# Kernel tuning notes

Measured on AMD Instinct MI355X. Metric: run time of the kernel, lower is better.

## Reference

```python
import jax, jax.numpy as jnp
import numpy as np

B, N, S, C, H = 16, 64, 4096, 384, 6
DH = C // H
SCALE = DH ** -0.5


def setup_inputs() -> dict:
    k0 = jax.random.key(0)
    ks = jax.random.split(k0, 7)
    std = C ** -0.5
    return {
        "query": jax.random.normal(ks[0], (B, N, C), jnp.float32),
        "key": jax.random.normal(ks[1], (B, S, C), jnp.float32),
        "Wq": jax.random.normal(ks[2], (C, C), jnp.float32) * std,
        "Wk": jax.random.normal(ks[3], (C, C), jnp.float32) * std,
        "Wv": jax.random.normal(ks[4], (C, C), jnp.float32) * std,
        "Wp": jax.random.normal(ks[5], (C, C), jnp.float32) * std,
        "bp": jnp.zeros((C,), jnp.float32),
    }


def reference(query, key, Wq, Wk, Wv, Wp, bp):
    # q/k/v projections (no bias, matching qkv_bias=False); nn.Linear is x @ W.T
    q = (query @ Wq.T).reshape(B, N, H, DH).transpose(0, 2, 1, 3)  # [B,H,N,DH]
    k = (key @ Wk.T).reshape(B, S, H, DH).transpose(0, 2, 1, 3)    # [B,H,S,DH]
    v = (key @ Wv.T).reshape(B, S, H, DH).transpose(0, 2, 1, 3)    # [B,H,S,DH]

    attn = jnp.einsum('bhnd,bhsd->bhns', q, k) * SCALE  # [B,H,N,S]

    # hard_softmax over dim=-2 (the group/query axis): each key token is
    # hard-assigned (straight-through) to its argmax group.
    y_soft = jax.nn.softmax(attn, axis=-2)
    idx = jnp.argmax(y_soft, axis=-2)  # [B,H,S]
    y_hard = (jnp.arange(N)[:, None] == idx[..., None, :]).astype(attn.dtype)  # [B,H,N,S]
    a = y_hard + y_soft - jax.lax.stop_gradient(y_soft)

    # inv_attn renormalization over the key axis
    a = a / (a.sum(axis=-1, keepdims=True) + 1.0)

    out = jnp.einsum('bhns,bhsd->bhnd', a, v)            # [B,H,N,DH]
    out = out.transpose(0, 2, 1, 3).reshape(B, N, C)     # [B,N,C]
    return out @ Wp.T + bp
```

## Files before the change

kernel.cpp:

```cpp
#include <hip/hip_runtime.h>
#include <hip/hip_bf16.h>
#include <stdint.h>

#define B_ 16
#define N_ 64
#define S_ 4096
#define C_ 384
#define H_ 6
#define DH_ 64
#define SCALE_ 0.125f
#define TAU_ 2e-4f
#define LISTCAP 262144

typedef __attribute__((ext_vector_type(8))) short bf16x8;
typedef __attribute__((ext_vector_type(4))) float f32x4;
typedef __attribute__((ext_vector_type(4))) unsigned short u16x4;

static __device__ __forceinline__ unsigned short f2bf(float x) {
    union { float f; unsigned u; } v; v.f = x;
    unsigned r = v.u + 0x7FFFu + ((v.u >> 16) & 1u);
    return (unsigned short)(r >> 16);
}
static __device__ __forceinline__ float bf2f(unsigned short b) {
    union { unsigned u; float f; } v; v.u = ((unsigned)b) << 16; return v.f;
}
static __device__ __forceinline__ float bfu_lo(unsigned u) {
    union { unsigned u; float f; } v; v.u = u << 16; return v.f;
}
static __device__ __forceinline__ float bfu_hi(unsigned u) {
    union { unsigned u; float f; } v; v.u = u & 0xFFFF0000u; return v.f;
}

static __device__ __forceinline__ void gl_lds16(const void* g, void* l) {
    __builtin_amdgcn_global_load_lds(
        (const __attribute__((address_space(1))) unsigned int*)g,
        (__attribute__((address_space(3))) unsigned int*)l, 16, 0, 0);
}

#define PREP_BLOCKS 8192
#define QK_BLOCKS   (8 * H_ * B_)
#define TR_BLOCKS   72

#define TRT(r, c) sbuf[(r) * 65 + (c)]
#define WQS(d, c) sbuf[(d) * 49 + (c)]

__global__ __launch_bounds__(384) void prepqk_kernel(const float* __restrict__ key,
                                                     unsigned short* __restrict__ khi,
                                                     unsigned short* __restrict__ klo,
                                                     const float* __restrict__ query,
                                                     const float* __restrict__ Wq,
                                                     const float* __restrict__ Wk,
                                                     float* __restrict__ qk,
                                                     unsigned short* __restrict__ qkhi,
                                                     unsigned short* __restrict__ qklo,
                                                     const float* __restrict__ Wp,
                                                     const float* __restrict__ Wv,
                                                     float* __restrict__ wpT,
                                                     float* __restrict__ wvT) {
    __shared__ float qstage[8][C_];
    __shared__ float qv[8][DH_];
    __shared__ float sbuf[64 * 65];
    int t = threadIdx.x;
    if (blockIdx.x < PREP_BLOCKS) {
        size_t blk = (size_t)blockIdx.x * 3072;
#pragma unroll
        for (int half = 0; half < 2; ++half) {
            size_t base = blk + (size_t)half * 1536 + (size_t)t * 4;
            float4 x = *(const float4*)(key + base);
            float xs[4] = { x.x, x.y, x.z, x.w };
            unsigned short hi[4], lo[4];
#pragma unroll
            for (int i = 0; i < 4; ++i) {
                hi[i] = f2bf(xs[i]);
                lo[i] = f2bf(xs[i] - bf2f(hi[i]));
            }
            *(u16x4*)(khi + base) = *(u16x4*)hi;
            *(u16x4*)(klo + base) = *(u16x4*)lo;
        }
        return;
    }
    int e = blockIdx.x - PREP_BLOCKS;
    if (e >= QK_BLOCKS) {
        int e2 = e - QK_BLOCKS;
        const float* src = (e2 < 36) ? Wp : Wv;
        float* dst = (e2 < 36) ? wpT : wvT;
        int tile = e2 % 36;
        int r0 = (tile / 6) * 64, c0 = (tile % 6) * 64;
        if (t < 256) {
#pragma unroll
            for (int rep = 0; rep < 16; ++rep) {
                int idx = rep * 256 + t;
                int r = idx >> 6, c = idx & 63;
                TRT(r, c) = src[(size_t)(r0 + r) * C_ + c0 + c];
            }
        }
        __syncthreads();
        if (t < 256) {
#pragma unroll
            for (int rep = 0; rep < 16; ++rep) {
                int idx = rep * 256 + t;
                int rT = idx >> 6, cT = idx & 63;
                dst[(size_t)(c0 + rT) * C_ + r0 + cT] = TRT(cT, rT);
            }
        }
        return;
    }
    int ng = e & 7;
    int h = (e >> 3) % H_;
    int b = e / (8 * H_);
    int n0 = ng * 8;
#pragma unroll
    for (int i = 0; i < 8; ++i)
        qstage[i][t] = query[((size_t)(b * N_ + n0 + i)) * C_ + t];
    {
        int i0 = (t < 256) ? (t >> 6) : 0;
        int d = t & 63;
        float accA = 0.f, accB = 0.f;
        for (int c0 = 0; c0 < C_; c0 += 48) {
            __syncthreads();
#pragma unroll
            for (int rep = 0; rep < 8; ++rep) {
                int idx2 = rep * 384 + t;
                int r = idx2 / 48, c = idx2 % 48;
                WQS(r, c) = Wq[(size_t)(h * DH_ + r) * C_ + c0 + c];
            }
            __syncthreads();
            if (t < 256) {
#pragma unroll
                for (int cc = 0; cc < 48; cc += 4) {
                    accA += qstage[i0][c0 + cc + 0] * WQS(d, cc + 0)
                          + qstage[i0][c0 + cc + 1] * WQS(d, cc + 1)
                          + qstage[i0][c0 + cc + 2] * WQS(d, cc + 2)
                          + qstage[i0][c0 + cc + 3] * WQS(d, cc + 3);
                    accB += qstage[i0 + 4][c0 + cc + 0] * WQS(d, cc + 0)
                          + qstage[i0 + 4][c0 + cc + 1] * WQS(d, cc + 1)
                          + qstage[i0 + 4][c0 + cc + 2] * WQS(d, cc + 2)
                          + qstage[i0 + 4][c0 + cc + 3] * WQS(d, cc + 3);
                }
            }
        }
        if (t < 256) {
            qv[i0][d] = accA * SCALE_;
            qv[i0 + 4][d] = accB * SCALE_;
        }
    }
    __syncthreads();
    float a[8];
#pragma unroll
    for (int i = 0; i < 8; ++i) a[i] = 0.f;
    {
        const float* wk = Wk + (size_t)h * DH_ * C_ + t;
#pragma unroll 4
        for (int d = 0; d < DH_; ++d) {
            float w = wk[(size_t)d * C_];
#pragma unroll
            for (int i = 0; i < 8; ++i) a[i] += qv[i][d] * w;
        }
    }
#pragma unroll
    for (int i = 0; i < 8; ++i) qstage[i][t] = a[i];
    __syncthreads();
    {
        int r = t / 48, c0 = (t % 48) * 8;
        float v[8];
#pragma unroll
        for (int j = 0; j < 8; ++j) v[j] = qstage[r][c0 + j];
        unsigned short hi[8], lo[8];
#pragma unroll
        for (int j = 0; j < 8; ++j) {
            hi[j] = f2bf(v[j]);
            lo[j] = f2bf(v[j] - bf2f(hi[j]));
        }
        size_t o = ((size_t)(b * H_ + h) * N_ + n0 + r) * C_ + c0;
        float4 f0 = { v[0], v[1], v[2], v[3] };
        float4 f1 = { v[4], v[5], v[6], v[7] };
        *(float4*)(qk + o) = f0;
        *(float4*)(qk + o + 4) = f1;
        *(bf16x8*)(qkhi + o) = *(bf16x8*)hi;
        *(bf16x8*)(qklo + o) = *(bf16x8*)lo;
    }
}

__global__ __launch_bounds__(256) void attn_kernel(const unsigned short* __restrict__ qkhi,
                                                   const unsigned short* __restrict__ qklo,
                                                   const unsigned short* __restrict__ khi,
                                                   const unsigned short* __restrict__ klo,
                                                   unsigned int* __restrict__ idx,
                                                   unsigned int* __restrict__ flag_cnt,
                                                   unsigned int* __restrict__ flag_list) {
    __shared__ __align__(16) unsigned short sAhi[64 * 32];
    __shared__ __align__(16) unsigned short sAlo[64 * 32];
    __shared__ __align__(16) unsigned short sBhi[128 * 32];
    __shared__ __align__(16) unsigned short sBlo[128 * 32];
    int tid = threadIdx.x;
    int w = tid >> 6, l = tid & 63;
    int wm = w >> 1, wn = w & 1;
    int q4 = l >> 4, lm = l & 15;
    int s0 = blockIdx.x * 128;
    int h = blockIdx.y, b = blockIdx.z;
    size_t kbK = ((size_t)b * S_ + s0) * C_;
    size_t kbA = (size_t)(b * H_ + h) * N_ * C_;
    int trow16 = l >> 2;
    int tquart = ((l & 3) ^ ((l >> 3) & 3)) * 8;
    int sw = (q4 ^ ((lm >> 1) & 3)) * 8;

    f32x4 acc[2][4];
#pragma unroll
    for (int tm = 0; tm < 2; ++tm)
#pragma unroll
        for (int nt = 0; nt < 4; ++nt) acc[tm][nt] = (f32x4)0.f;

    for (int kc = 0; kc < C_; kc += 32) {
        __syncthreads();
#pragma unroll
        for (int i = 0; i < 6; ++i) {
            int gid = w * 6 + i;
            if (gid < 8) {
                gl_lds16(khi + kbK + (size_t)(gid * 16 + trow16) * C_ + kc + tquart,
                         (char*)sBhi + gid * 1024);
            } else if (gid < 16) {
                int g2 = gid - 8;
                gl_lds16(klo + kbK + (size_t)(g2 * 16 + trow16) * C_ + kc + tquart,
                         (char*)sBlo + g2 * 1024);
            } else if (gid < 20) {
                int g2 = gid - 16;
                gl_lds16(qkhi + kbA + (size_t)(g2 * 16 + trow16) * C_ + kc + tquart,
                         (char*)sAhi + g2 * 1024);
            } else {
                int g2 = gid - 20;
                gl_lds16(qklo + kbA + (size_t)(g2 * 16 + trow16) * C_ + kc + tquart,
                         (char*)sAlo + g2 * 1024);
            }
        }
        __syncthreads();
        bf16x8 ah[2], al[2];
#pragma unroll
        for (int tm = 0; tm < 2; ++tm) {
            int ar = (wm * 32 + tm * 16 + lm) * 32 + sw;
            ah[tm] = *(const bf16x8*)&sAhi[ar];
            al[tm] = *(const bf16x8*)&sAlo[ar];
        }
#pragma unroll
        for (int nt = 0; nt < 4; ++nt) {
            int nr = ((wn * 4 + nt) * 16 + lm) * 32 + sw;
            bf16x8 bh = *(const bf16x8*)&sBhi[nr];
            bf16x8 bl = *(const bf16x8*)&sBlo[nr];
#pragma unroll
            for (int tm = 0; tm < 2; ++tm) {
                acc[tm][nt] = __builtin_amdgcn_mfma_f32_16x16x32_bf16(ah[tm], bh, acc[tm][nt], 0, 0, 0);
                acc[tm][nt] = __builtin_amdgcn_mfma_f32_16x16x32_bf16(ah[tm], bl, acc[tm][nt], 0, 0, 0);
                acc[tm][nt] = __builtin_amdgcn_mfma_f32_16x16x32_bf16(al[tm], bh, acc[tm][nt], 0, 0, 0);
            }
        }
    }
    __syncthreads();

    float* rm1 = (float*)sBhi;
    float* rm2 = rm1 + 256;
    int* ri1 = (int*)(rm2 + 256);
    int* ri2 = ri1 + 256;

#pragma unroll
    for (int nt = 0; nt < 4; ++nt) {
        float m1 = -3.4e38f, m2 = -3.4e38f; int i1 = 0, i2 = 0;
#pragma unroll
        for (int tm = 0; tm < 2; ++tm)
#pragma unroll
            for (int r = 0; r < 4; ++r) {
                float v = acc[tm][nt][r];
                int row = wm * 32 + tm * 16 + q4 * 4 + r;
                if (v > m1) { m2 = m1; i2 = i1; m1 = v; i1 = row; }
                else if (v > m2) { m2 = v; i2 = row; }
            }
#pragma unroll
        for (int off = 16; off < 64; off <<= 1) {
            float om1 = __shfl_xor(m1, off), om2 = __shfl_xor(m2, off);
            int oi1 = __shfl_xor(i1, off), oi2 = __shfl_xor(i2, off);
            bool take = (om1 > m1) || (om1 == m1 && oi1 < i1);
            float w1 = take ? om1 : m1; int wi1 = take ? oi1 : i1;
            float l1 = take ? m1 : om1; int li1 = take ? i1 : oi1;
            float s2 = m2; int si2 = i2;
            if (om2 > s2) { s2 = om2; si2 = oi2; }
            if (l1 > s2) { s2 = l1; si2 = li1; }
            m1 = w1; i1 = wi1; m2 = s2; i2 = si2;
        }
        if (q4 == 0) {
            int cw = (wn * 4 + nt) * 16 + lm;
            rm1[wm * 128 + cw] = m1; rm2[wm * 128 + cw] = m2;
            ri1[wm * 128 + cw] = i1; ri2[wm * 128 + cw] = i2;
        }
    }
    __syncthreads();
    if (tid < 128) {
        float a1 = rm1[tid], a2 = rm2[tid];
        int ai1 = ri1[tid], ai2 = ri2[tid];
        float b1 = rm1[128 + tid], b2 = rm2[128 + tid];
        int bi1 = ri1[128 + tid], bi2 = ri2[128 + tid];
        float w1, s2; int wi1, wi2;
        if (b1 > a1) { w1 = b1; wi1 = bi1; s2 = a1; wi2 = ai1; if (b2 > s2) { s2 = b2; wi2 = bi2; } }
        else         { w1 = a1; wi1 = ai1; s2 = a2; wi2 = ai2; if (b1 > s2) { s2 = b1; wi2 = bi1; } }
        idx[(size_t)(b * H_ + h) * S_ + s0 + tid] = (unsigned)wi1;
        if (w1 - s2 < TAU_) {
            unsigned p = atomicAdd(flag_cnt, 1u);
            if (p < LISTCAP) {
                unsigned tok = (unsigned)((b * H_ + h) * S_ + s0 + tid);
                flag_list[p] = tok | ((unsigned)wi1 << 19) | ((unsigned)wi2 << 25);
            }
        }
    }
}

__global__ __launch_bounds__(256) void fixup_kernel(const float* __restrict__ qk,
                                                    const float* __restrict__ key,
                                                    const unsigned int* __restrict__ flag_list,
                                                    const unsigned int* __restrict__ flag_cnt,
                                                    unsigned int* __restrict__ idx) {
    int w = threadIdx.x >> 6, l = threadIdx.x & 63;
    unsigned total = flag_cnt[0];
    if (total > LISTCAP) total = LISTCAP;
    for (unsigned t = blockIdx.x * 4 + w; t < total; t += gridDim.x * 4) {
        unsigned e = flag_list[t];
        unsigned tok = e & 0x7FFFFu;
        int i1 = (int)((e >> 19) & 63u), i2 = (int)((e >> 25) & 63u);
        unsigned bh = tok >> 12;
        unsigned s = tok & 4095u;
        unsigned bb = bh / H_;
        int l32 = l & 31;
        const float* qrow = qk + ((size_t)bh * N_ + (l < 32 ? i1 : i2)) * C_ + l32 * 12;
        const float* krow = key + ((size_t)bb * S_ + s) * C_ + l32 * 12;
        float sum = 0.f;
#pragma unroll
        for (int c = 0; c < 12; ++c) sum += qrow[c] * krow[c];
#pragma unroll
        for (int off = 1; off < 32; off <<= 1) sum += __shfl_xor(sum, off);
        float d1 = __shfl(sum, 0);
        float d2 = __shfl(sum, 32);
        int win = (d2 > d1 || (d2 == d1 && i2 < i1)) ? i2 : i1;
        if (l == 0) idx[(size_t)bh * S_ + s] = (unsigned)win;
    }
}

__global__ __launch_bounds__(256) void hist_build_kernel(const unsigned int* __restrict__ idx,
                                                         unsigned int* __restrict__ offs,
                                                         unsigned int* __restrict__ order) {
    __shared__ unsigned int cnts[N_];
    __shared__ unsigned int pos[N_];
    int tid = threadIdx.x;
    int bh = blockIdx.x;
    if (tid < N_) cnts[tid] = 0u;
    __syncthreads();
    const unsigned int* idxp = idx + (size_t)bh * S_;
    for (int s = tid; s < S_; s += 256) atomicAdd(&cnts[idxp[s]], 1u);
    __syncthreads();
    if (tid < N_) {
        unsigned v = cnts[tid];
        unsigned x = v;
#pragma unroll
        for (int off = 1; off < 64; off <<= 1) {
            unsigned y = __shfl_up(x, off);
            if (tid >= off) x += y;
        }
        unsigned excl = x - v;
        pos[tid] = excl;
        offs[(size_t)bh * 65 + tid] = excl;
        if (tid == 63) offs[(size_t)bh * 65 + 64] = x;
    }
    __syncthreads();
    unsigned int* op = order + (size_t)bh * S_;
    for (int s = tid; s < S_; s += 256) {
        unsigned g = idxp[s];
        unsigned p = atomicAdd(&pos[g], 1u);
        op[p] = (unsigned)s;
    }
}

#define AGG_PARTS 8
__global__ __launch_bounds__(512) void aggv_kernel(const unsigned short* __restrict__ khi,
                                                   const unsigned int* __restrict__ order,
                                                   const unsigned int* __restrict__ offs,
                                                   const float* __restrict__ wvT,
                                                   float* __restrict__ gvn) {
    __shared__ float lrows[AGG_PARTS][C_];
    __shared__ float zrow[C_];
    __shared__ float pacc[AGG_PARTS][DH_];
    int tid = threadIdx.x;
    int part = tid >> 6, l = tid & 63;
    int h = blockIdx.y, b = blockIdx.z;
    int bh = b * H_ + h;
    int g = blockIdx.x;
    unsigned beg = offs[(size_t)bh * 65 + g];
    unsigned end = offs[(size_t)bh * 65 + g + 1];
    int cnt = (int)(end - beg);
    float inv = 1.f / ((float)cnt + 1.f);
    const unsigned int* op = order + (size_t)bh * S_ + beg;
    const unsigned int* kbase = (const unsigned int*)(khi + (size_t)b * S_ * C_);
    float a0 = 0.f, a1 = 0.f, a2 = 0.f, a3 = 0.f, a4 = 0.f, a5 = 0.f;
    for (int base = part * 64; base < cnt; base += 64 * AGG_PARTS) {
        int m = cnt - base; if (m > 64) m = 64;
        unsigned sv = (l < m) ? op[base + l] : 0u;
        int i = 0;
        for (; i + 8 <= m; i += 8) {
            int ss[8];
#pragma unroll
            for (int j = 0; j < 8; ++j) ss[j] = __shfl((int)sv, i + j);
            unsigned u[8][3];
#pragma unroll
            for (int j = 0; j < 8; ++j) {
                const unsigned int* kp = kbase + (size_t)ss[j] * (C_ / 2) + l * 3;
                u[j][0] = kp[0]; u[j][1] = kp[1]; u[j][2] = kp[2];
            }
#pragma unroll
            for (int j = 0; j < 8; ++j) {
                a0 += bfu_lo(u[j][0]); a1 += bfu_hi(u[j][0]);
                a2 += bfu_lo(u[j][1]); a3 += bfu_hi(u[j][1]);
                a4 += bfu_lo(u[j][2]); a5 += bfu_hi(u[j][2]);
            }
        }
        for (; i < m; ++i) {
            int s = (int)__shfl((int)sv, i);
            const unsigned int* kp = kbase + (size_t)s * (C_ / 2) + l * 3;
            unsigned u0 = kp[0], u1 = kp[1], u2 = kp[2];
            a0 += bfu_lo(u0); a1 += bfu_hi(u0);
            a2 += bfu_lo(u1); a3 += bfu_hi(u1);
            a4 += bfu_lo(u2); a5 += bfu_hi(u2);
        }
    }
    float* lp = &lrows[part][l * 6];
    lp[0] = a0 * inv; lp[1] = a1 * inv; lp[2] = a2 * inv;
    lp[3] = a3 * inv; lp[4] = a4 * inv; lp[5] = a5 * inv;
    __syncthreads();
    if (tid < C_) {
        float z = lrows[0][tid];
#pragma unroll
        for (int p = 1; p < AGG_PARTS; ++p) z += lrows[p][tid];
        zrow[tid] = z;
    }
    __syncthreads();
    {
        float a = 0.f;
        int cb = part * (C_ / AGG_PARTS);
#pragma unroll 8
        for (int cc = 0; cc < C_ / AGG_PARTS; ++cc) {
            int c = cb + cc;
            a += zrow[c] * wvT[(size_t)c * C_ + h * DH_ + l];
        }
        pacc[part][l] = a;
    }
    __syncthreads();
    if (part == 0) {
        float acc = pacc[0][l];
#pragma unroll
        for (int p = 1; p < AGG_PARTS; ++p) acc += pacc[p][l];
        gvn[((size_t)bh * N_ + g) * DH_ + l] = acc;
    }
}

__global__ __launch_bounds__(384) void out_kernel(const float* __restrict__ gvn,
                                                  const float* __restrict__ wpT,
                                                  const float* __restrict__ bp,
                                                  float* __restrict__ out) {
    __shared__ float vals[C_];
    int bn = blockIdx.x;
    int b = bn >> 6, n = bn & 63;
    int t = threadIdx.x;
    int h = t >> 6, d = t & 63;
    vals[t] = gvn[((size_t)(b * H_ + h) * N_ + n) * DH_ + d];
    __syncthreads();
    float s = bp[t];
#pragma unroll 8
    for (int c = 0; c < C_; ++c)
        s += vals[c] * wpT[(size_t)c * C_ + t];
    out[(size_t)bn * C_ + t] = s;
}

extern "C" void kernel_launch(void* const* d_in, const int* in_sizes, int n_in,
                              void* d_out, int out_size, void* d_ws, size_t ws_size,
                              hipStream_t stream) {
    (void)in_sizes; (void)n_in; (void)out_size; (void)ws_size;
    const float* query = (const float*)d_in[0];
    const float* key   = (const float*)d_in[1];
    const float* Wq    = (const float*)d_in[2];
    const float* Wk    = (const float*)d_in[3];
    const float* Wv    = (const float*)d_in[4];
    const float* Wp    = (const float*)d_in[5];
    const float* bp    = (const float*)d_in[6];
    float* out = (float*)d_out;

    char* ws = (char*)d_ws;
    size_t off = 0;
    unsigned short* khi  = (unsigned short*)(ws + off); off += (size_t)B_ * S_ * C_ * 2;
    unsigned short* klo  = (unsigned short*)(ws + off); off += (size_t)B_ * S_ * C_ * 2;
    float* qk            = (float*)(ws + off);          off += (size_t)B_ * H_ * N_ * C_ * 4;
    unsigned short* qkhi = (unsigned short*)(ws + off); off += (size_t)B_ * H_ * N_ * C_ * 2;
    unsigned short* qklo = (unsigned short*)(ws + off); off += (size_t)B_ * H_ * N_ * C_ * 2;
    unsigned int* idx    = (unsigned int*)(ws + off);   off += (size_t)B_ * H_ * S_ * 4;
    unsigned int* order  = (unsigned int*)(ws + off);   off += (size_t)B_ * H_ * S_ * 4;
    unsigned int* offs   = (unsigned int*)(ws + off);   off += (size_t)B_ * H_ * 65 * 4;
    float* gvn           = (float*)(ws + off);          off += (size_t)B_ * H_ * N_ * DH_ * 4;
    float* wpT           = (float*)(ws + off);          off += (size_t)C_ * C_ * 4;
    float* wvT           = (float*)(ws + off);          off += (size_t)C_ * C_ * 4;
    unsigned int* fcnt   = (unsigned int*)(ws + off);   off += 256;
    unsigned int* flist  = (unsigned int*)(ws + off);   off += (size_t)LISTCAP * 4;

    hipMemsetAsync(fcnt, 0, 256, stream);

    prepqk_kernel<<<PREP_BLOCKS + QK_BLOCKS + TR_BLOCKS, 384, 0, stream>>>(
        key, khi, klo, query, Wq, Wk, qk, qkhi, qklo, Wp, Wv, wpT, wvT);
    attn_kernel<<<dim3(S_ / 128, H_, B_), 256, 0, stream>>>(qkhi, qklo, khi, klo, idx, fcnt, flist);
    fixup_kernel<<<256, 256, 0, stream>>>(qk, key, flist, fcnt, idx);
    hist_build_kernel<<<B_ * H_, 256, 0, stream>>>(idx, offs, order);
    aggv_kernel<<<dim3(N_, H_, B_), 512, 0, stream>>>(khi, order, offs, wvT, gvn);
    out_kernel<<<B_ * N_, 384, 0, stream>>>(gvn, wpT, bp, out);
}
```

Baseline: 377.7 us.

## Fuse key bf16 hi/lo split into attention kernel, drop key prep pass

Result: no change. 384.1 us (+1.7%).

```diff
diff --git a/kernel.cpp b/kernel.cpp
--- a/kernel.cpp
+++ b/kernel.cpp
@@ -14,7 +14,6 @@
 
 typedef __attribute__((ext_vector_type(8))) short bf16x8;
 typedef __attribute__((ext_vector_type(4))) float f32x4;
-typedef __attribute__((ext_vector_type(4))) unsigned short u16x4;
 
 static __device__ __forceinline__ unsigned short f2bf(float x) {
     union { float f; unsigned u; } v; v.f = x;
@@ -24,12 +23,6 @@
 static __device__ __forceinline__ float bf2f(unsigned short b) {
     union { unsigned u; float f; } v; v.u = ((unsigned)b) << 16; return v.f;
 }
-static __device__ __forceinline__ float bfu_lo(unsigned u) {
-    union { unsigned u; float f; } v; v.u = u << 16; return v.f;
-}
-static __device__ __forceinline__ float bfu_hi(unsigned u) {
-    union { unsigned u; float f; } v; v.u = u & 0xFFFF0000u; return v.f;
-}
 
 static __device__ __forceinline__ void gl_lds16(const void* g, void* l) {
     __builtin_amdgcn_global_load_lds(
@@ -37,49 +30,27 @@
         (__attribute__((address_space(3))) unsigned int*)l, 16, 0, 0);
 }
 
-#define PREP_BLOCKS 8192
 #define QK_BLOCKS   (8 * H_ * B_)
 #define TR_BLOCKS   72
 
 #define TRT(r, c) sbuf[(r) * 65 + (c)]
 #define WQS(d, c) sbuf[(d) * 49 + (c)]
 
-__global__ __launch_bounds__(384) void prepqk_kernel(const float* __restrict__ key,
-                                                     unsigned short* __restrict__ khi,
-                                                     unsigned short* __restrict__ klo,
-                                                     const float* __restrict__ query,
-                                                     const float* __restrict__ Wq,
-                                                     const float* __restrict__ Wk,
-                                                     float* __restrict__ qk,
-                                                     unsigned short* __restrict__ qkhi,
-                                                     unsigned short* __restrict__ qklo,
-                                                     const float* __restrict__ Wp,
-                                                     const float* __restrict__ Wv,
-                                                     float* __restrict__ wpT,
-                                                     float* __restrict__ wvT) {
+__global__ __launch_bounds__(384) void qkT_kernel(const float* __restrict__ query,
+                                                  const float* __restrict__ Wq,
+                                                  const float* __restrict__ Wk,
+                                                  float* __restrict__ qk,
+                                                  unsigned short* __restrict__ qkhi,
+                                                  unsigned short* __restrict__ qklo,
+                                                  const float* __restrict__ Wp,
+                                                  const float* __restrict__ Wv,
+                                                  float* __restrict__ wpT,
+                                                  float* __restrict__ wvT) {
     __shared__ float qstage[8][C_];
     __shared__ float qv[8][DH_];
     __shared__ float sbuf[64 * 65];
     int t = threadIdx.x;
-    if (blockIdx.x < PREP_BLOCKS) {
-        size_t blk = (size_t)blockIdx.x * 3072;
-#pragma unroll
-        for (int half = 0; half < 2; ++half) {
-            size_t base = blk + (size_t)half * 1536 + (size_t)t * 4;
-            float4 x = *(const float4*)(key + base);
-            float xs[4] = { x.x, x.y, x.z, x.w };
-            unsigned short hi[4], lo[4];
-#pragma unroll
-            for (int i = 0; i < 4; ++i) {
-                hi[i] = f2bf(xs[i]);
-                lo[i] = f2bf(xs[i] - bf2f(hi[i]));
-            }
-            *(u16x4*)(khi + base) = *(u16x4*)hi;
-            *(u16x4*)(klo + base) = *(u16x4*)lo;
-        }
-        return;
-    }
-    int e = blockIdx.x - PREP_BLOCKS;
+    int e = blockIdx.x;
     if (e >= QK_BLOCKS) {
         int e2 = e - QK_BLOCKS;
         const float* src = (e2 < 36) ? Wp : Wv;
@@ -183,15 +154,13 @@
 
 __global__ __launch_bounds__(256) void attn_kernel(const unsigned short* __restrict__ qkhi,
                                                    const unsigned short* __restrict__ qklo,
-                                                   const unsigned short* __restrict__ khi,
-                                                   const unsigned short* __restrict__ klo,
+                                                   const float* __restrict__ key,
                                                    unsigned int* __restrict__ idx,
                                                    unsigned int* __restrict__ flag_cnt,
                                                    unsigned int* __restrict__ flag_list) {
+    __shared__ __align__(16) float sB[128 * 32];
     __shared__ __align__(16) unsigned short sAhi[64 * 32];
     __shared__ __align__(16) unsigned short sAlo[64 * 32];
-    __shared__ __align__(16) unsigned short sBhi[128 * 32];
-    __shared__ __align__(16) unsigned short sBlo[128 * 32];
     int tid = threadIdx.x;
     int w = tid >> 6, l = tid & 63;
     int wm = w >> 1, wn = w & 1;
@@ -203,6 +172,9 @@
     int trow16 = l >> 2;
     int tquart = ((l & 3) ^ ((l >> 3) & 3)) * 8;
     int sw = (q4 ^ ((lm >> 1) & 3)) * 8;
+    int swrow = l >> 3;
+    int swcol = ((l & 7) ^ (l >> 3)) * 4;
+    int sx = (lm & 7) << 4;
 
     f32x4 acc[2][4];
 #pragma unroll
@@ -215,13 +187,9 @@
 #pragma unroll
         for (int i = 0; i < 6; ++i) {
             int gid = w * 6 + i;
-            if (gid < 8) {
-                gl_lds16(khi + kbK + (size_t)(gid * 16 + trow16) * C_ + kc + tquart,
-                         (char*)sBhi + gid * 1024);
-            } else if (gid < 16) {
-                int g2 = gid - 8;
-                gl_lds16(klo + kbK + (size_t)(g2 * 16 + trow16) * C_ + kc + tquart,
-                         (char*)sBlo + g2 * 1024);
+            if (gid < 16) {
+                gl_lds16(key + kbK + (size_t)(gid * 8 + swrow) * C_ + kc + swcol,
+                         (char*)sB + gid * 1024);
             } else if (gid < 20) {
                 int g2 = gid - 16;
                 gl_lds16(qkhi + kbA + (size_t)(g2 * 16 + trow16) * C_ + kc + tquart,
@@ -242,9 +210,19 @@
         }
 #pragma unroll
         for (int nt = 0; nt < 4; ++nt) {
-            int nr = ((wn * 4 + nt) * 16 + lm) * 32 + sw;
-            bf16x8 bh = *(const bf16x8*)&sBhi[nr];
-            bf16x8 bl = *(const bf16x8*)&sBlo[nr];
+            int tr = (wn * 4 + nt) * 16 + lm;
+            const char* rowb = (const char*)sB + tr * 128;
+            float4 x0 = *(const float4*)(rowb + ((q4 * 32) ^ sx));
+            float4 x1 = *(const float4*)(rowb + ((q4 * 32 + 16) ^ sx));
+            float xs[8] = { x0.x, x0.y, x0.z, x0.w, x1.x, x1.y, x1.z, x1.w };
+            unsigned short hh[8], ll[8];
+#pragma unroll
+            for (int j = 0; j < 8; ++j) {
+                hh[j] = f2bf(xs[j]);
+                ll[j] = f2bf(xs[j] - bf2f(hh[j]));
+            }
+            bf16x8 bh = *(bf16x8*)hh;
+            bf16x8 bl = *(bf16x8*)ll;
 #pragma unroll
             for (int tm = 0; tm < 2; ++tm) {
                 acc[tm][nt] = __builtin_amdgcn_mfma_f32_16x16x32_bf16(ah[tm], bh, acc[tm][nt], 0, 0, 0);
@@ -255,7 +233,7 @@
     }
     __syncthreads();
 
-    float* rm1 = (float*)sBhi;
+    float* rm1 = (float*)sB;
     float* rm2 = rm1 + 256;
     int* ri1 = (int*)(rm2 + 256);
     int* ri2 = ri1 + 256;
@@ -340,9 +318,9 @@
     }
 }
 
-__global__ __launch_bounds__(256) void hist_build_kernel(const unsigned int* __restrict__ idx,
-                                                         unsigned int* __restrict__ offs,
-                                                         unsigned int* __restrict__ order) {
+__global__ __launch_bounds__(1024) void hist_build_kernel(const unsigned int* __restrict__ idx,
+                                                          unsigned int* __restrict__ offs,
+                                                          unsigned int* __restrict__ order) {
     __shared__ unsigned int cnts[N_];
     __shared__ unsigned int pos[N_];
     int tid = threadIdx.x;
@@ -350,7 +328,7 @@
     if (tid < N_) cnts[tid] = 0u;
     __syncthreads();
     const unsigned int* idxp = idx + (size_t)bh * S_;
-    for (int s = tid; s < S_; s += 256) atomicAdd(&cnts[idxp[s]], 1u);
+    for (int s = tid; s < S_; s += 1024) atomicAdd(&cnts[idxp[s]], 1u);
     __syncthreads();
     if (tid < N_) {
         unsigned v = cnts[tid];
@@ -367,7 +345,7 @@
     }
     __syncthreads();
     unsigned int* op = order + (size_t)bh * S_;
-    for (int s = tid; s < S_; s += 256) {
+    for (int s = tid; s < S_; s += 1024) {
         unsigned g = idxp[s];
         unsigned p = atomicAdd(&pos[g], 1u);
         op[p] = (unsigned)s;
@@ -375,7 +353,7 @@
 }
 
 #define AGG_PARTS 8
-__global__ __launch_bounds__(512) void aggv_kernel(const unsigned short* __restrict__ khi,
+__global__ __launch_bounds__(512) void aggv_kernel(const float* __restrict__ key,
                                                    const unsigned int* __restrict__ order,
                                                    const unsigned int* __restrict__ offs,
                                                    const float* __restrict__ wvT,
@@ -393,7 +371,7 @@
     int cnt = (int)(end - beg);
     float inv = 1.f / ((float)cnt + 1.f);
     const unsigned int* op = order + (size_t)bh * S_ + beg;
-    const unsigned int* kbase = (const unsigned int*)(khi + (size_t)b * S_ * C_);
+    const float* kbase = key + (size_t)b * S_ * C_;
     float a0 = 0.f, a1 = 0.f, a2 = 0.f, a3 = 0.f, a4 = 0.f, a5 = 0.f;
     for (int base = part * 64; base < cnt; base += 64 * AGG_PARTS) {
         int m = cnt - base; if (m > 64) m = 64;
@@ -403,26 +381,29 @@
             int ss[8];
 #pragma unroll
             for (int j = 0; j < 8; ++j) ss[j] = __shfl((int)sv, i + j);
-            unsigned u[8][3];
+            float2 u[8][3];
 #pragma unroll
             for (int j = 0; j < 8; ++j) {
-                const unsigned int* kp = kbase + (size_t)ss[j] * (C_ / 2) + l * 3;
-                u[j][0] = kp[0]; u[j][1] = kp[1]; u[j][2] = kp[2];
+                const float* kp = kbase + (size_t)ss[j] * C_ + l * 6;
+                u[j][0] = *(const float2*)kp;
+                u[j][1] = *(const float2*)(kp + 2);
+                u[j][2] = *(const float2*)(kp + 4);
             }
 #pragma unroll
             for (int j = 0; j < 8; ++j) {
-                a0 += bfu_lo(u[j][0]); a1 += bfu_hi(u[j][0]);
-                a2 += bfu_lo(u[j][1]); a3 += bfu_hi(u[j][1]);
-                a4 += bfu_lo(u[j][2]); a5 += bfu_hi(u[j][2]);
+                a0 += u[j][0].x; a1 += u[j][0].y;
+                a2 += u[j][1].x; a3 += u[j][1].y;
+                a4 += u[j][2].x; a5 += u[j][2].y;
             }
         }
         for (; i < m; ++i) {
             int s = (int)__shfl((int)sv, i);
-            const unsigned int* kp = kbase + (size_t)s * (C_ / 2) + l * 3;
-            unsigned u0 = kp[0], u1 = kp[1], u2 = kp[2];
-            a0 += bfu_lo(u0); a1 += bfu_hi(u0);
-            a2 += bfu_lo(u1); a3 += bfu_hi(u1);
-            a4 += bfu_lo(u2); a5 += bfu_hi(u2);
+            const float* kp = kbase + (size_t)s * C_ + l * 6;
+            float2 u0 = *(const float2*)kp;
+            float2 u1 = *(const float2*)(kp + 2);
+            float2 u2 = *(const float2*)(kp + 4);
+            a0 += u0.x; a1 += u0.y; a2 += u1.x;
+            a3 += u1.y; a4 += u2.x; a5 += u2.y;
         }
     }
     float* lp = &lrows[part][l * 6];
@@ -488,8 +469,6 @@
 
     char* ws = (char*)d_ws;
     size_t off = 0;
-    unsigned short* khi  = (unsigned short*)(ws + off); off += (size_t)B_ * S_ * C_ * 2;
-    unsigned short* klo  = (unsigned short*)(ws + off); off += (size_t)B_ * S_ * C_ * 2;
     float* qk            = (float*)(ws + off);          off += (size_t)B_ * H_ * N_ * C_ * 4;
     unsigned short* qkhi = (unsigned short*)(ws + off); off += (size_t)B_ * H_ * N_ * C_ * 2;
     unsigned short* qklo = (unsigned short*)(ws + off); off += (size_t)B_ * H_ * N_ * C_ * 2;
@@ -504,11 +483,11 @@
 
     hipMemsetAsync(fcnt, 0, 256, stream);
 
-    prepqk_kernel<<<PREP_BLOCKS + QK_BLOCKS + TR_BLOCKS, 384, 0, stream>>>(
-        key, khi, klo, query, Wq, Wk, qk, qkhi, qklo, Wp, Wv, wpT, wvT);
-    attn_kernel<<<dim3(S_ / 128, H_, B_), 256, 0, stream>>>(qkhi, qklo, khi, klo, idx, fcnt, flist);
+    qkT_kernel<<<QK_BLOCKS + TR_BLOCKS, 384, 0, stream>>>(
+        query, Wq, Wk, qk, qkhi, qklo, Wp, Wv, wpT, wvT);
+    attn_kernel<<<dim3(S_ / 128, H_, B_), 256, 0, stream>>>(qkhi, qklo, key, idx, fcnt, flist);
     fixup_kernel<<<256, 256, 0, stream>>>(qk, key, flist, fcnt, idx);
-    hist_build_kernel<<<B_ * H_, 256, 0, stream>>>(idx, offs, order);
-    aggv_kernel<<<dim3(N_, H_, B_), 512, 0, stream>>>(khi, order, offs, wvT, gvn);
+    hist_build_kernel<<<B_ * H_, 1024, 0, stream>>>(idx, offs, order);
+    aggv_kernel<<<dim3(N_, H_, B_), 512, 0, stream>>>(key, order, offs, wvT, gvn);
     out_kernel<<<B_ * N_, 384, 0, stream>>>(gvn, wpT, bp, out);
 }
```

## Double-buffer LDS tiles in attention score kernel to overlap loads with MFMA

Applied to the files above, without the earlier changes.

Result: no change. 373.8 us (-1.0%).

```diff
diff --git a/kernel.cpp b/kernel.cpp
--- a/kernel.cpp
+++ b/kernel.cpp
@@ -188,10 +188,10 @@
                                                    unsigned int* __restrict__ idx,
                                                    unsigned int* __restrict__ flag_cnt,
                                                    unsigned int* __restrict__ flag_list) {
-    __shared__ __align__(16) unsigned short sAhi[64 * 32];
-    __shared__ __align__(16) unsigned short sAlo[64 * 32];
-    __shared__ __align__(16) unsigned short sBhi[128 * 32];
-    __shared__ __align__(16) unsigned short sBlo[128 * 32];
+    __shared__ __align__(16) unsigned short sAhi[2][64 * 32];
+    __shared__ __align__(16) unsigned short sAlo[2][64 * 32];
+    __shared__ __align__(16) unsigned short sBhi[2][128 * 32];
+    __shared__ __align__(16) unsigned short sBlo[2][128 * 32];
     int tid = threadIdx.x;
     int w = tid >> 6, l = tid & 63;
     int wm = w >> 1, wn = w & 1;
@@ -210,41 +210,50 @@
 #pragma unroll
         for (int nt = 0; nt < 4; ++nt) acc[tm][nt] = (f32x4)0.f;
 
-    for (int kc = 0; kc < C_; kc += 32) {
-        __syncthreads();
-#pragma unroll
-        for (int i = 0; i < 6; ++i) {
-            int gid = w * 6 + i;
-            if (gid < 8) {
-                gl_lds16(khi + kbK + (size_t)(gid * 16 + trow16) * C_ + kc + tquart,
-                         (char*)sBhi + gid * 1024);
-            } else if (gid < 16) {
-                int g2 = gid - 8;
-                gl_lds16(klo + kbK + (size_t)(g2 * 16 + trow16) * C_ + kc + tquart,
-                         (char*)sBlo + g2 * 1024);
-            } else if (gid < 20) {
-                int g2 = gid - 16;
-                gl_lds16(qkhi + kbA + (size_t)(g2 * 16 + trow16) * C_ + kc + tquart,
-                         (char*)sAhi + g2 * 1024);
-            } else {
-                int g2 = gid - 20;
-                gl_lds16(qklo + kbA + (size_t)(g2 * 16 + trow16) * C_ + kc + tquart,
-                         (char*)sAlo + g2 * 1024);
-            }
-        }
-        __syncthreads();
+#define STAGE(buf, kc)                                                                   \
+    do {                                                                                 \
+        _Pragma("unroll")                                                                \
+        for (int i_ = 0; i_ < 6; ++i_) {                                                 \
+            int gid = w * 6 + i_;                                                        \
+            if (gid < 8) {                                                               \
+                gl_lds16(khi + kbK + (size_t)(gid * 16 + trow16) * C_ + (kc) + tquart,   \
+                         (char*)sBhi[buf] + gid * 1024);                                 \
+            } else if (gid < 16) {                                                       \
+                int g2 = gid - 8;                                                        \
+                gl_lds16(klo + kbK + (size_t)(g2 * 16 + trow16) * C_ + (kc) + tquart,    \
+                         (char*)sBlo[buf] + g2 * 1024);                                  \
+            } else if (gid < 20) {                                                       \
+                int g2 = gid - 16;                                                       \
+                gl_lds16(qkhi + kbA + (size_t)(g2 * 16 + trow16) * C_ + (kc) + tquart,   \
+                         (char*)sAhi[buf] + g2 * 1024);                                  \
+            } else {                                                                     \
+                int g2 = gid - 20;                                                       \
+                gl_lds16(qklo + kbA + (size_t)(g2 * 16 + trow16) * C_ + (kc) + tquart,   \
+                         (char*)sAlo[buf] + g2 * 1024);                                  \
+            }                                                                            \
+        }                                                                                \
+    } while (0)
+
+    STAGE(0, 0);
+    asm volatile("s_waitcnt vmcnt(0)" ::: "memory");
+    __builtin_amdgcn_s_barrier();
+
+    for (int t = 0; t < C_ / 32; ++t) {
+        int cur = t & 1;
+        if (t + 1 < C_ / 32) STAGE(cur ^ 1, (t + 1) * 32);
+
         bf16x8 ah[2], al[2];
 #pragma unroll
         for (int tm = 0; tm < 2; ++tm) {
             int ar = (wm * 32 + tm * 16 + lm) * 32 + sw;
-            ah[tm] = *(const bf16x8*)&sAhi[ar];
-            al[tm] = *(const bf16x8*)&sAlo[ar];
+            ah[tm] = *(const bf16x8*)&sAhi[cur][ar];
+            al[tm] = *(const bf16x8*)&sAlo[cur][ar];
         }
 #pragma unroll
         for (int nt = 0; nt < 4; ++nt) {
             int nr = ((wn * 4 + nt) * 16 + lm) * 32 + sw;
-            bf16x8 bh = *(const bf16x8*)&sBhi[nr];
-            bf16x8 bl = *(const bf16x8*)&sBlo[nr];
+            bf16x8 bh = *(const bf16x8*)&sBhi[cur][nr];
+            bf16x8 bl = *(const bf16x8*)&sBlo[cur][nr];
 #pragma unroll
             for (int tm = 0; tm < 2; ++tm) {
                 acc[tm][nt] = __builtin_amdgcn_mfma_f32_16x16x32_bf16(ah[tm], bh, acc[tm][nt], 0, 0, 0);
@@ -252,7 +261,11 @@
                 acc[tm][nt] = __builtin_amdgcn_mfma_f32_16x16x32_bf16(al[tm], bh, acc[tm][nt], 0, 0, 0);
             }
         }
-    }
+        asm volatile("s_waitcnt vmcnt(0) lgkmcnt(0)" ::: "memory");
+        __builtin_amdgcn_sched_barrier(0);
+        __builtin_amdgcn_s_barrier();
+    }
+#undef STAGE
     __syncthreads();
 
     float* rm1 = (float*)sBhi;
```
